# Kernel optimization log

Hardware: AMD Instinct MI355X
Metric: run time of the kernel (lower is better)

## Reference

```python
import jax, jax.numpy as jnp
import numpy as np
from jax import lax

B, X, H, W, C = 4, 32, 8, 128, 32  # batch, frames, height, width, channels (dim)


def setup_inputs() -> dict:
    key = jax.random.key(0)
    k1, k2, k3, k4, k5, k6 = jax.random.split(key, 6)
    return {
        "storage": jax.random.normal(k1, (B, X, H, W, C), jnp.float32),
        "target": jax.random.normal(k2, (B, 1, H, W, C), jnp.float32),
        # Conv3d(dim, 2*dim, kernel=(3,1,1), padding=(1,0,0)) weight/bias
        "w_cross": jax.random.normal(k3, (2 * C, C, 3, 1, 1), jnp.float32) * 0.05,
        "b_cross": jax.random.normal(k4, (2 * C,), jnp.float32) * 0.05,
        # Conv2d(dim, dim, kernel=1) weight (stored as [out, in]) / bias
        "w_q": jax.random.normal(k5, (C, C), jnp.float32) * 0.1,
        "b_q": jax.random.normal(k6, (C,), jnp.float32) * 0.1,
    }


def reference(storage, target, w_cross, b_cross, w_q, b_q):
    # storage [B,X,H,W,C] -> transpose(4,1).transpose(4,2) -> [B,C,X,W,H]
    s = jnp.transpose(storage, (0, 4, 1, 3, 2))
    # target [B,1,H,W,C] -> transpose(4,2) -> [B,1,C,W,H] -> squeeze(1) -> [B,C,W,H]
    t = jnp.transpose(target, (0, 1, 4, 3, 2))[:, 0]

    # Conv3d over the X (depth) axis, kernel (3,1,1), padding (1,0,0)
    out = lax.conv_general_dilated(
        s, w_cross, window_strides=(1, 1, 1),
        padding=((1, 1), (0, 0), (0, 0)),
        dimension_numbers=("NCDHW", "OIDHW", "NCDHW"),
    ) + b_cross[None, :, None, None, None]          # [B,2C,X,W,H]
    s_v, s_k = jnp.split(out, 2, axis=1)            # each [B,C,X,W,H]

    # 1x1 Conv2d query projection
    t_q = jnp.einsum("oc,bcwh->bowh", w_q, t) + b_q[None, :, None, None]  # [B,C,W,H]
    # unsqueeze(1).transpose(2,1).repeat over X -> [B,C,X,W,H]
    t_q = jnp.broadcast_to(t_q[:, :, None], (B, C, X, W, H))

    # Faithful torch .view on contiguous [B,C,X,W,H]: row-major reshape mixes C into last dim
    t_q = t_q.reshape(B, X * W, C * H)
    s_v = s_v.reshape(B, X * W, C * H)
    s_k = jnp.swapaxes(s_k.reshape(B, X * W, C * H), 1, 2)  # [B, C*H, X*W]

    kq = jax.nn.softmax(jnp.einsum("bnc,bcm->bnm", t_q, s_k), axis=-1)  # [B, XW, XW]
    final = jnp.einsum("bnm,bmc->bnc", kq, s_v)                          # [B, XW, C*H]
    return final.reshape(B, X, H, W, C)
```

## Files before the change

### kernel.cpp

```cpp
#include <hip/hip_runtime.h>

typedef unsigned short u16;
typedef unsigned int u32;
typedef __attribute__((ext_vector_type(8))) short s16x8;
typedef __attribute__((ext_vector_type(4))) float f32x4;

#define WS_A      0u
#define WS_B      8388608u
#define WS_C      16777216u
#define WS_D      25165824u
#define WS_E      25427968u
#define WS_LP     25452544u
#define WS_NEEDED 25485312u

__device__ __forceinline__ u16 f2bf(float f){
  u32 u = __float_as_uint(f);
  return (u16)((u + 0x7fffu + ((u >> 16) & 1u)) >> 16);
}

__global__ __launch_bounds__(256) void zero_out_kernel(float* __restrict__ out){
  int t = blockIdx.x * 256 + threadIdx.x;
  ((float4*)out)[t] = make_float4(0.f, 0.f, 0.f, 0.f);
}

__global__ __launch_bounds__(256) void prep_kernel(const float* __restrict__ target,
    const float* __restrict__ w_q, const float* __restrict__ b_q, u16* __restrict__ Qbf,
    const float* __restrict__ w_cross, float* __restrict__ wT){
  int bid = blockIdx.x;
  int tid = threadIdx.x;
  if (bid >= 512){
    int t = (bid - 512) * 256 + tid;
    wT[t] = w_cross[(t & 63) * 96 + (t >> 6)];
    return;
  }
  int wc = bid & 3;
  int cq = (bid >> 2) & 31;
  int b  = bid >> 7;
  int wl = tid & 31, h = tid >> 5;
  int w = wc * 32 + wl;
  float in[32];
  const float4* p = (const float4*)(target + (((size_t)b*8 + h)*128 + w)*32);
  #pragma unroll
  for (int q = 0; q < 8; ++q){
    float4 v = p[q];
    in[q*4+0] = v.x; in[q*4+1] = v.y; in[q*4+2] = v.z; in[q*4+3] = v.w;
  }
  float acc = b_q[cq];
  #pragma unroll
  for (int c = 0; c < 32; ++c) acc += in[c] * w_q[cq*32 + c];
  __shared__ float stg[256];
  stg[wl*8 + h] = acc;
  __syncthreads();
  Qbf[((size_t)b*128 + cq*4 + wc)*256 + tid] = f2bf(stg[tid]);
}

__global__ __launch_bounds__(256, 2) void conv_kernel(const float* __restrict__ storage,
    const float* __restrict__ wT, const float* __restrict__ b_cross,
    u16* __restrict__ Kb, u16* __restrict__ Vb){
  int bid = blockIdx.x;
  int wc  = bid & 3;
  int x   = (bid >> 2) & 31;
  int og2 = (bid >> 7) & 3;
  int b   = bid >> 9;
  int tid = threadIdx.x;
  int wl = tid & 31, h = tid >> 5;
  int w = wc * 32 + wl;
  int obase_ch = og2 * 16;

  float acc[16];
  #pragma unroll
  for (int i = 0; i < 16; ++i) acc[i] = b_cross[obase_ch + i];

  #pragma unroll
  for (int dx = 0; dx < 3; ++dx){
    int xx = x + dx - 1;
    if (xx < 0 || xx > 31) continue;
    float vv[32];
    const float4* p = (const float4*)(storage + ((((size_t)b*32 + xx)*8 + h)*128 + w)*32);
    #pragma unroll
    for (int q = 0; q < 8; ++q){
      float4 v = p[q];
      vv[q*4+0] = v.x; vv[q*4+1] = v.y; vv[q*4+2] = v.z; vv[q*4+3] = v.w;
    }
    #pragma unroll
    for (int c = 0; c < 32; ++c){
      float v = vv[c];
      const float* wp = wT + (c*3 + dx)*64 + obase_ch;
      #pragma unroll
      for (int i = 0; i < 16; ++i) acc[i] = fmaf(v, wp[i], acc[i]);
    }
  }

  int m = wl*8 + h;
  size_t base = ((size_t)b*4096 + (size_t)x*4 + wc)*256 + m;
  if (og2 < 2){
    #pragma unroll
    for (int i = 0; i < 16; ++i)
      Vb[base + (size_t)(obase_ch + i)*32768] = f2bf(acc[i]);
  } else {
    #pragma unroll
    for (int i = 0; i < 16; ++i)
      Kb[base + (size_t)(obase_ch + i - 32)*32768] = f2bf(acc[i]);
  }
}

__global__ __launch_bounds__(256, 2) void flash_kernel(const u16* __restrict__ Qbf,
    const u16* __restrict__ Kb, const u16* __restrict__ Vb,
    float* __restrict__ Opart, float* __restrict__ lpart){
  int kq = blockIdx.x & 15, rb = (blockIdx.x >> 4) & 7, b = blockIdx.x >> 7;
  int tid = threadIdx.x;
  int w = tid >> 6, lane = tid & 63, l15 = lane & 15, quad = lane >> 4;

  __shared__ alignas(16) u16 Vts[256 * 64];
  __shared__ alignas(16) u16 Ps[16 * 64];
  __shared__ float lsumW[64];

  s16x8 qa[8];
  {
    const u16* qp = Qbf + ((size_t)(b*128 + rb*16 + l15))*256 + quad*8;
    #pragma unroll
    for (int ks = 0; ks < 8; ++ks) qa[ks] = *(const s16x8*)(qp + ks*32);
  }

  int jl4 = tid & 15, mseg = tid >> 4;
  const u16* kbase = Kb + ((size_t)(b*4096 + kq*256 + w*16 + l15))*256 + quad*8;
  const u16* vbase = Vb + ((size_t)(b*4096 + kq*256 + jl4*4))*256 + mseg*16;

  s16x8 kr[8];
  #pragma unroll
  for (int ks = 0; ks < 8; ++ks) kr[ks] = *(const s16x8*)(kbase + ks*32);
  u32 kv[4][8];
  #pragma unroll
  for (int kk = 0; kk < 4; ++kk){
    uint4 a = *(const uint4*)(vbase + kk*256);
    uint4 b2 = *(const uint4*)(vbase + kk*256 + 8);
    kv[kk][0]=a.x; kv[kk][1]=a.y; kv[kk][2]=a.z; kv[kk][3]=a.w;
    kv[kk][4]=b2.x; kv[kk][5]=b2.y; kv[kk][6]=b2.z; kv[kk][7]=b2.w;
  }

  float lacc[4] = {0.f, 0.f, 0.f, 0.f};
  f32x4 oc[4];
  #pragma unroll
  for (int mt = 0; mt < 4; ++mt) oc[mt] = (f32x4){0.f,0.f,0.f,0.f};

  #pragma unroll
  for (int it = 0; it < 4; ++it){
    if (it > 0) __syncthreads();

    #pragma unroll
    for (int i = 0; i < 16; ++i){
      int d = i >> 1;
      u32 e0, e1, e2, e3;
      if (i & 1){ e0 = kv[0][d] >> 16;     e1 = kv[1][d] >> 16;
                  e2 = kv[2][d] >> 16;     e3 = kv[3][d] >> 16; }
      else      { e0 = kv[0][d] & 0xffffu; e1 = kv[1][d] & 0xffffu;
                  e2 = kv[2][d] & 0xffffu; e3 = kv[3][d] & 0xffffu; }
      int m = mseg*16 + i;
      int col = (((jl4 >> 1) ^ (m & 7)) << 3) + ((jl4 & 1) << 2);
      *(uint2*)&Vts[m*64 + col] = make_uint2(e0 | (e1 << 16), e2 | (e3 << 16));
    }

    f32x4 s0 = {0.f,0.f,0.f,0.f}, s1 = {0.f,0.f,0.f,0.f};
    #pragma unroll
    for (int ks = 0; ks < 8; ks += 2){
      s0 = __builtin_amdgcn_mfma_f32_16x16x32_bf16(qa[ks],   kr[ks],   s0, 0, 0, 0);
      s1 = __builtin_amdgcn_mfma_f32_16x16x32_bf16(qa[ks+1], kr[ks+1], s1, 0, 0, 0);
    }
    int b8k = w*2 + (l15 >> 3);
    #pragma unroll
    for (int reg = 0; reg < 4; ++reg){
      float sv = fminf(s0[reg] + s1[reg], 80.f);
      float p = __expf(sv);
      int row = quad*4 + reg;
      Ps[row*64 + ((b8k ^ (row & 7)) << 3) + (l15 & 7)] = f2bf(p);
      lacc[reg] += p;
    }

    if (it < 3){
      const u16* vp = vbase + (it+1)*16384;
      #pragma unroll
      for (int kk = 0; kk < 4; ++kk){
        uint4 a = *(const uint4*)(vp + kk*256);
        uint4 b2 = *(const uint4*)(vp + kk*256 + 8);
        kv[kk][0]=a.x; kv[kk][1]=a.y; kv[kk][2]=a.z; kv[kk][3]=a.w;
        kv[kk][4]=b2.x; kv[kk][5]=b2.y; kv[kk][6]=b2.z; kv[kk][7]=b2.w;
      }
    }
    __syncthreads();

    if (it < 3){
      const u16* kp = kbase + (it+1)*16384;
      #pragma unroll
      for (int ks = 0; ks < 8; ++ks) kr[ks] = *(const s16x8*)(kp + ks*32);
    }
    #pragma unroll
    for (int ks2 = 0; ks2 < 2; ++ks2){
      int b8 = ks2*4 + quad;
      s16x8 pb = *(const s16x8*)&Ps[l15*64 + ((b8 ^ (l15 & 7)) << 3)];
      #pragma unroll
      for (int mt = 0; mt < 4; ++mt){
        int mrow = (w*4 + mt)*16 + l15;
        s16x8 af = *(const s16x8*)&Vts[mrow*64 + ((b8 ^ (mrow & 7)) << 3)];
        oc[mt] = __builtin_amdgcn_mfma_f32_16x16x32_bf16(af, pb, oc[mt], 0, 0, 0);
      }
    }
  }

  #pragma unroll
  for (int reg = 0; reg < 4; ++reg){
    float t = lacc[reg];
    t += __shfl_xor(t, 1); t += __shfl_xor(t, 2);
    t += __shfl_xor(t, 4); t += __shfl_xor(t, 8);
    lacc[reg] = t;
  }
  if (l15 == 0){
    #pragma unroll
    for (int reg = 0; reg < 4; ++reg) lsumW[w*16 + quad*4 + reg] = lacc[reg];
  }
  __syncthreads();
  if (tid < 16)
    lpart[(b*16 + kq)*128 + rb*16 + tid] =
        lsumW[tid] + lsumW[16 + tid] + lsumW[32 + tid] + lsumW[48 + tid];
  {
    float* dst = Opart + ((size_t)((b*16 + kq)*128 + rb*16 + l15))*256 + w*64 + quad*4;
    #pragma unroll
    for (int mt = 0; mt < 4; ++mt)
      *(float4*)(dst + mt*16) = make_float4(oc[mt][0], oc[mt][1], oc[mt][2], oc[mt][3]);
  }
}

__global__ __launch_bounds__(256) void combine_kernel(const float* __restrict__ lpart,
    const float* __restrict__ Opart, float* __restrict__ out){
  int r = blockIdx.x & 127, b = blockIdx.x >> 7;
  int m = threadIdx.x;
  float L = 0.f, o = 0.f;
  #pragma unroll
  for (int kq = 0; kq < 16; ++kq){
    L += lpart[(b*16 + kq)*128 + r];
    o += Opart[((size_t)((b*16 + kq)*128 + r))*256 + m];
  }
  o /= L;
  int cq = r >> 2, whi = r & 3;
  size_t obase = ((size_t)b*32 + cq) * 32768;
  #pragma unroll
  for (int hh = 0; hh < 8; ++hh){
    #pragma unroll
    for (int wt = 0; wt < 4; ++wt){
      out[obase + hh*4096 + wt*1024 + whi*256 + m] = o;
    }
  }
}

extern "C" void kernel_launch(void* const* d_in, const int* in_sizes, int n_in,
                              void* d_out, int out_size, void* d_ws, size_t ws_size,
                              hipStream_t stream){
  const float* storage = (const float*)d_in[0];
  const float* target  = (const float*)d_in[1];
  const float* w_cross = (const float*)d_in[2];
  const float* b_cross = (const float*)d_in[3];
  const float* w_q     = (const float*)d_in[4];
  const float* b_q     = (const float*)d_in[5];
  float* out = (float*)d_out;

  if (ws_size < (size_t)WS_NEEDED){
    zero_out_kernel<<<dim3(4096), dim3(256), 0, stream>>>(out);
    return;
  }

  char* ws = (char*)d_ws;
  float* Opart = (float*)(ws + WS_A);
  u16*   Kb    = (u16*)(ws + WS_B);
  u16*   Vb    = (u16*)(ws + WS_C);
  u16*   Qbf   = (u16*)(ws + WS_D);
  float* wT    = (float*)(ws + WS_E);
  float* lpart = (float*)(ws + WS_LP);

  prep_kernel    <<<dim3(536),  dim3(256), 0, stream>>>(target, w_q, b_q, Qbf, w_cross, wT);
  conv_kernel    <<<dim3(2048), dim3(256), 0, stream>>>(storage, wT, b_cross, Kb, Vb);
  flash_kernel   <<<dim3(512),  dim3(256), 0, stream>>>(Qbf, Kb, Vb, Opart, lpart);
  combine_kernel <<<dim3(512),  dim3(256), 0, stream>>>(lpart, Opart, out);
}
```

Before: 135.8 us.

## Fuse four stage kernels into one cooperative persistent kernel with grid syncs

Moves the prep, conv, flash and combine stages into device-function bodies and runs them from a single cooperative mega-kernel. A persistent grid, sized from the occupancy query and capped at 512 blocks, loops over each stage's work units, with grid.sync between stages. This removes three kernel launch boundaries and their idle gaps. In exchange it adds grid-wide barrier cost, an occupancy query on the host at every call, possible lower parallelism in the conv stage (2048 units on at most 512 blocks), and register pressure from merging all stages into one kernel. The old four-kernel path stays as a fallback if the cooperative launch fails.

```diff
diff --git a/kernel.cpp b/kernel.cpp
--- a/kernel.cpp
+++ b/kernel.cpp
@@ -1,4 +1,7 @@
 #include <hip/hip_runtime.h>
+#include <hip/hip_cooperative_groups.h>
+
+namespace cg = cooperative_groups;
 
 typedef unsigned short u16;
 typedef unsigned int u32;
@@ -23,16 +26,10 @@
   ((float4*)out)[t] = make_float4(0.f, 0.f, 0.f, 0.f);
 }
 
-__global__ __launch_bounds__(256) void prep_kernel(const float* __restrict__ target,
-    const float* __restrict__ w_q, const float* __restrict__ b_q, u16* __restrict__ Qbf,
-    const float* __restrict__ w_cross, float* __restrict__ wT){
-  int bid = blockIdx.x;
-  int tid = threadIdx.x;
-  if (bid >= 512){
-    int t = (bid - 512) * 256 + tid;
-    wT[t] = w_cross[(t & 63) * 96 + (t >> 6)];
-    return;
-  }
+
+__device__ __forceinline__ void qproj_body(int bid, int tid,
+    const float* __restrict__ target, const float* __restrict__ w_q,
+    const float* __restrict__ b_q, u16* __restrict__ Qbf, float* stg){
   int wc = bid & 3;
   int cq = (bid >> 2) & 31;
   int b  = bid >> 7;
@@ -48,21 +45,18 @@
   float acc = b_q[cq];
   #pragma unroll
   for (int c = 0; c < 32; ++c) acc += in[c] * w_q[cq*32 + c];
-  __shared__ float stg[256];
   stg[wl*8 + h] = acc;
   __syncthreads();
   Qbf[((size_t)b*128 + cq*4 + wc)*256 + tid] = f2bf(stg[tid]);
 }
 
-__global__ __launch_bounds__(256, 2) void conv_kernel(const float* __restrict__ storage,
-    const float* __restrict__ wT, const float* __restrict__ b_cross,
-    u16* __restrict__ Kb, u16* __restrict__ Vb){
-  int bid = blockIdx.x;
+__device__ __forceinline__ void conv_body(int bid, int tid,
+    const float* __restrict__ storage, const float* __restrict__ wT,
+    const float* __restrict__ b_cross, u16* __restrict__ Kb, u16* __restrict__ Vb){
   int wc  = bid & 3;
   int x   = (bid >> 2) & 31;
   int og2 = (bid >> 7) & 3;
   int b   = bid >> 9;
-  int tid = threadIdx.x;
   int wl = tid & 31, h = tid >> 5;
   int w = wc * 32 + wl;
   int obase_ch = og2 * 16;
@@ -104,16 +98,16 @@
   }
 }
 
-__global__ __launch_bounds__(256, 2) void flash_kernel(const u16* __restrict__ Qbf,
-    const u16* __restrict__ Kb, const u16* __restrict__ Vb,
-    float* __restrict__ Opart, float* __restrict__ lpart){
-  int kq = blockIdx.x & 15, rb = (blockIdx.x >> 4) & 7, b = blockIdx.x >> 7;
-  int tid = threadIdx.x;
+__device__ __forceinline__ void flash_body(int bid, int tid,
+    const u16* __restrict__ Qbf, const u16* __restrict__ Kb,
+    const u16* __restrict__ Vb, float* __restrict__ Opart,
+    float* __restrict__ lpart, char* smem){
+  u16*   Vts   = (u16*)smem;
+  u16*   Ps    = (u16*)(smem + 32768);
+  float* lsumW = (float*)(smem + 34816);
+
+  int kq = bid & 15, rb = (bid >> 4) & 7, b = bid >> 7;
   int w = tid >> 6, lane = tid & 63, l15 = lane & 15, quad = lane >> 4;
-
-  __shared__ alignas(16) u16 Vts[256 * 64];
-  __shared__ alignas(16) u16 Ps[16 * 64];
-  __shared__ float lsumW[64];
 
   s16x8 qa[8];
   {
@@ -145,7 +139,7 @@
 
   #pragma unroll
   for (int it = 0; it < 4; ++it){
-    if (it > 0) __syncthreads();
+    __syncthreads();
 
     #pragma unroll
     for (int i = 0; i < 16; ++i){
@@ -213,6 +207,7 @@
     t += __shfl_xor(t, 4); t += __shfl_xor(t, 8);
     lacc[reg] = t;
   }
+  __syncthreads();
   if (l15 == 0){
     #pragma unroll
     for (int reg = 0; reg < 4; ++reg) lsumW[w*16 + quad*4 + reg] = lacc[reg];
@@ -229,10 +224,11 @@
   }
 }
 
-__global__ __launch_bounds__(256) void combine_kernel(const float* __restrict__ lpart,
-    const float* __restrict__ Opart, float* __restrict__ out){
-  int r = blockIdx.x & 127, b = blockIdx.x >> 7;
-  int m = threadIdx.x;
+__device__ __forceinline__ void combine_body(int bid, int tid,
+    const float* __restrict__ lpart, const float* __restrict__ Opart,
+    float* __restrict__ out){
+  int r = bid & 127, b = bid >> 7;
+  int m = tid;
   float L = 0.f, o = 0.f;
   #pragma unroll
   for (int kq = 0; kq < 16; ++kq){
@@ -249,6 +245,81 @@
       out[obase + hh*4096 + wt*1024 + whi*256 + m] = o;
     }
   }
+}
+
+
+__global__ __launch_bounds__(256) void prep_kernel(const float* __restrict__ target,
+    const float* __restrict__ w_q, const float* __restrict__ b_q, u16* __restrict__ Qbf,
+    const float* __restrict__ w_cross, float* __restrict__ wT){
+  __shared__ float stg[256];
+  int bid = blockIdx.x, tid = threadIdx.x;
+  if (bid >= 512){
+    int t = (bid - 512) * 256 + tid;
+    wT[t] = w_cross[(t & 63) * 96 + (t >> 6)];
+    return;
+  }
+  qproj_body(bid, tid, target, w_q, b_q, Qbf, stg);
+}
+
+__global__ __launch_bounds__(256, 2) void conv_kernel(const float* __restrict__ storage,
+    const float* __restrict__ wT, const float* __restrict__ b_cross,
+    u16* __restrict__ Kb, u16* __restrict__ Vb){
+  conv_body(blockIdx.x, threadIdx.x, storage, wT, b_cross, Kb, Vb);
+}
+
+__global__ __launch_bounds__(256, 2) void flash_kernel(const u16* __restrict__ Qbf,
+    const u16* __restrict__ Kb, const u16* __restrict__ Vb,
+    float* __restrict__ Opart, float* __restrict__ lpart){
+  __shared__ alignas(16) char smem[35072];
+  flash_body(blockIdx.x, threadIdx.x, Qbf, Kb, Vb, Opart, lpart, smem);
+}
+
+__global__ __launch_bounds__(256) void combine_kernel(const float* __restrict__ lpart,
+    const float* __restrict__ Opart, float* __restrict__ out){
+  combine_body(blockIdx.x, threadIdx.x, lpart, Opart, out);
+}
+
+
+__global__ __launch_bounds__(256, 2) void mega_kernel(
+    const float* __restrict__ storage, const float* __restrict__ target,
+    const float* __restrict__ w_cross, const float* __restrict__ b_cross,
+    const float* __restrict__ w_q, const float* __restrict__ b_q,
+    float* __restrict__ out, char* __restrict__ ws){
+  cg::grid_group grid = cg::this_grid();
+
+  float* Opart = (float*)(ws + WS_A);
+  u16*   Kb    = (u16*)(ws + WS_B);
+  u16*   Vb    = (u16*)(ws + WS_C);
+  u16*   Qbf   = (u16*)(ws + WS_D);
+  float* wT    = (float*)(ws + WS_E);
+  float* lpart = (float*)(ws + WS_LP);
+
+  __shared__ alignas(16) char smem[35072];
+
+  int tid = threadIdx.x;
+  int G = gridDim.x;
+
+  for (int u = blockIdx.x; u < 536; u += G){
+    if (u >= 512){
+      int t = (u - 512)*256 + tid;
+      wT[t] = w_cross[(t & 63) * 96 + (t >> 6)];
+    } else {
+      qproj_body(u, tid, target, w_q, b_q, Qbf, (float*)smem);
+    }
+    __syncthreads();
+  }
+  grid.sync();
+
+  for (int u = blockIdx.x; u < 2048; u += G)
+    conv_body(u, tid, storage, wT, b_cross, Kb, Vb);
+  grid.sync();
+
+  for (int u = blockIdx.x; u < 512; u += G)
+    flash_body(u, tid, Qbf, Kb, Vb, Opart, lpart, smem);
+  grid.sync();
+
+  for (int u = blockIdx.x; u < 512; u += G)
+    combine_body(u, tid, lpart, Opart, out);
 }
 
 extern "C" void kernel_launch(void* const* d_in, const int* in_sizes, int n_in,
@@ -261,22 +332,37 @@
   const float* w_q     = (const float*)d_in[4];
   const float* b_q     = (const float*)d_in[5];
   float* out = (float*)d_out;
+  char* ws = (char*)d_ws;
 
   if (ws_size < (size_t)WS_NEEDED){
     zero_out_kernel<<<dim3(4096), dim3(256), 0, stream>>>(out);
     return;
   }
 
-  char* ws = (char*)d_ws;
-  float* Opart = (float*)(ws + WS_A);
-  u16*   Kb    = (u16*)(ws + WS_B);
-  u16*   Vb    = (u16*)(ws + WS_C);
-  u16*   Qbf   = (u16*)(ws + WS_D);
-  float* wT    = (float*)(ws + WS_E);
-  float* lpart = (float*)(ws + WS_LP);
-
-  prep_kernel    <<<dim3(536),  dim3(256), 0, stream>>>(target, w_q, b_q, Qbf, w_cross, wT);
-  conv_kernel    <<<dim3(2048), dim3(256), 0, stream>>>(storage, wT, b_cross, Kb, Vb);
-  flash_kernel   <<<dim3(512),  dim3(256), 0, stream>>>(Qbf, Kb, Vb, Opart, lpart);
-  combine_kernel <<<dim3(512),  dim3(256), 0, stream>>>(lpart, Opart, out);
-}
+  bool coop_ok = false;
+  int occ = 0;
+  hipError_t qerr = hipOccupancyMaxActiveBlocksPerMultiprocessor(
+      &occ, (const void*)mega_kernel, 256, 0);
+  if (qerr == hipSuccess && occ > 0){
+    int grid = occ * 256;
+    if (grid > 512) grid = 512;
+    void* args[] = {(void*)&storage, (void*)&target, (void*)&w_cross, (void*)&b_cross,
+                    (void*)&w_q, (void*)&b_q, (void*)&out, (void*)&ws};
+    hipError_t lerr = hipLaunchCooperativeKernel((const void*)mega_kernel,
+                                                 dim3(grid), dim3(256), args, 0, stream);
+    coop_ok = (lerr == hipSuccess);
+  }
+  if (!coop_ok){
+    (void)hipGetLastError();
+    float* Opart = (float*)(ws + WS_A);
+    u16*   Kb    = (u16*)(ws + WS_B);
+    u16*   Vb    = (u16*)(ws + WS_C);
+    u16*   Qbf   = (u16*)(ws + WS_D);
+    float* wT    = (float*)(ws + WS_E);
+    float* lpart = (float*)(ws + WS_LP);
+    prep_kernel    <<<dim3(536),  dim3(256), 0, stream>>>(target, w_q, b_q, Qbf, w_cross, wT);
+    conv_kernel    <<<dim3(2048), dim3(256), 0, stream>>>(storage, wT, b_cross, Kb, Vb);
+    flash_kernel   <<<dim3(512),  dim3(256), 0, stream>>>(Qbf, Kb, Vb, Opart, lpart);
+    combine_kernel <<<dim3(512),  dim3(256), 0, stream>>>(lpart, Opart, out);
+  }
+}
```

Result: slower. 309.9 us (+128.1%).

## Fuse query projection into conv kernel and drop weight transpose pass

Applied to the files above, without the earlier changes.

Merges the prep kernel (query projection plus conv-weight transpose) into the conv kernel, so the first 512 blocks also compute Q, and reads w_cross directly in its original layout instead of a transposed copy. Each thread now loads all three input frames up front (96 registers) and loops over output channels without unrolling, storing each result as soon as it is computed. This removes one kernel launch and the wT workspace, at the cost of higher register pressure and strided weight reads. A __syncthreads is also added before the lsum shared-memory write in the flash kernel.

```diff
diff --git a/kernel.cpp b/kernel.cpp
--- a/kernel.cpp
+++ b/kernel.cpp
@@ -9,7 +9,6 @@
 #define WS_B      8388608u
 #define WS_C      16777216u
 #define WS_D      25165824u
-#define WS_E      25427968u
 #define WS_LP     25452544u
 #define WS_NEEDED 25485312u
 
@@ -23,84 +22,77 @@
   ((float4*)out)[t] = make_float4(0.f, 0.f, 0.f, 0.f);
 }
 
-__global__ __launch_bounds__(256) void prep_kernel(const float* __restrict__ target,
-    const float* __restrict__ w_q, const float* __restrict__ b_q, u16* __restrict__ Qbf,
-    const float* __restrict__ w_cross, float* __restrict__ wT){
+__global__ __launch_bounds__(256, 2) void convq_kernel(const float* __restrict__ storage,
+    const float* __restrict__ target, const float* __restrict__ w_cross,
+    const float* __restrict__ b_cross, const float* __restrict__ w_q,
+    const float* __restrict__ b_q, u16* __restrict__ Kb, u16* __restrict__ Vb,
+    u16* __restrict__ Qbf){
   int bid = blockIdx.x;
   int tid = threadIdx.x;
-  if (bid >= 512){
-    int t = (bid - 512) * 256 + tid;
-    wT[t] = w_cross[(t & 63) * 96 + (t >> 6)];
-    return;
-  }
-  int wc = bid & 3;
-  int cq = (bid >> 2) & 31;
-  int b  = bid >> 7;
   int wl = tid & 31, h = tid >> 5;
-  int w = wc * 32 + wl;
-  float in[32];
-  const float4* p = (const float4*)(target + (((size_t)b*8 + h)*128 + w)*32);
-  #pragma unroll
-  for (int q = 0; q < 8; ++q){
-    float4 v = p[q];
-    in[q*4+0] = v.x; in[q*4+1] = v.y; in[q*4+2] = v.z; in[q*4+3] = v.w;
-  }
-  float acc = b_q[cq];
-  #pragma unroll
-  for (int c = 0; c < 32; ++c) acc += in[c] * w_q[cq*32 + c];
-  __shared__ float stg[256];
-  stg[wl*8 + h] = acc;
-  __syncthreads();
-  Qbf[((size_t)b*128 + cq*4 + wc)*256 + tid] = f2bf(stg[tid]);
-}
-
-__global__ __launch_bounds__(256, 2) void conv_kernel(const float* __restrict__ storage,
-    const float* __restrict__ wT, const float* __restrict__ b_cross,
-    u16* __restrict__ Kb, u16* __restrict__ Vb){
-  int bid = blockIdx.x;
-  int wc  = bid & 3;
-  int x   = (bid >> 2) & 31;
-  int og2 = (bid >> 7) & 3;
-  int b   = bid >> 9;
-  int tid = threadIdx.x;
-  int wl = tid & 31, h = tid >> 5;
-  int w = wc * 32 + wl;
-  int obase_ch = og2 * 16;
-
-  float acc[16];
-  #pragma unroll
-  for (int i = 0; i < 16; ++i) acc[i] = b_cross[obase_ch + i];
-
-  #pragma unroll
-  for (int dx = 0; dx < 3; ++dx){
-    int xx = x + dx - 1;
-    if (xx < 0 || xx > 31) continue;
-    float vv[32];
-    const float4* p = (const float4*)(storage + ((((size_t)b*32 + xx)*8 + h)*128 + w)*32);
+
+  if (bid < 512){
+    int wc = bid & 3;
+    int cq = (bid >> 2) & 31;
+    int b  = bid >> 7;
+    int w = wc * 32 + wl;
+    float in[32];
+    const float4* p = (const float4*)(target + (((size_t)b*8 + h)*128 + w)*32);
     #pragma unroll
     for (int q = 0; q < 8; ++q){
       float4 v = p[q];
-      vv[q*4+0] = v.x; vv[q*4+1] = v.y; vv[q*4+2] = v.z; vv[q*4+3] = v.w;
-    }
-    #pragma unroll
-    for (int c = 0; c < 32; ++c){
-      float v = vv[c];
-      const float* wp = wT + (c*3 + dx)*64 + obase_ch;
-      #pragma unroll
-      for (int i = 0; i < 16; ++i) acc[i] = fmaf(v, wp[i], acc[i]);
-    }
-  }
-
-  int m = wl*8 + h;
-  size_t base = ((size_t)b*4096 + (size_t)x*4 + wc)*256 + m;
-  if (og2 < 2){
-    #pragma unroll
-    for (int i = 0; i < 16; ++i)
-      Vb[base + (size_t)(obase_ch + i)*32768] = f2bf(acc[i]);
-  } else {
-    #pragma unroll
-    for (int i = 0; i < 16; ++i)
-      Kb[base + (size_t)(obase_ch + i - 32)*32768] = f2bf(acc[i]);
+      in[q*4+0] = v.x; in[q*4+1] = v.y; in[q*4+2] = v.z; in[q*4+3] = v.w;
+    }
+    float acc = b_q[cq];
+    #pragma unroll
+    for (int c = 0; c < 32; ++c) acc += in[c] * w_q[cq*32 + c];
+    __shared__ float stg[256];
+    stg[wl*8 + h] = acc;
+    __syncthreads();
+    Qbf[((size_t)b*128 + cq*4 + wc)*256 + tid] = f2bf(stg[tid]);
+  }
+
+  {
+    int wc  = bid & 3;
+    int x   = (bid >> 2) & 31;
+    int og2 = (bid >> 7) & 3;
+    int b   = bid >> 9;
+    int w = wc * 32 + wl;
+    int obase_ch = og2 * 16;
+
+    float vv[3][32];
+    #pragma unroll
+    for (int dx = 0; dx < 3; ++dx){
+      int xx = x + dx - 1;
+      if (xx < 0 || xx > 31){
+        #pragma unroll
+        for (int c = 0; c < 32; ++c) vv[dx][c] = 0.f;
+      } else {
+        const float4* p = (const float4*)(storage + ((((size_t)b*32 + xx)*8 + h)*128 + w)*32);
+        #pragma unroll
+        for (int q = 0; q < 8; ++q){
+          float4 v = p[q];
+          vv[dx][q*4+0] = v.x; vv[dx][q*4+1] = v.y;
+          vv[dx][q*4+2] = v.z; vv[dx][q*4+3] = v.w;
+        }
+      }
+    }
+
+    int m = wl*8 + h;
+    size_t base = ((size_t)b*4096 + (size_t)x*4 + wc)*256 + m;
+    #pragma unroll 1
+    for (int i = 0; i < 16; ++i){
+      int o = obase_ch + i;
+      const float* wp = w_cross + o*96;
+      float acc = b_cross[o];
+      #pragma unroll
+      for (int c = 0; c < 32; ++c){
+        acc += vv[0][c]*wp[c*3+0] + vv[1][c]*wp[c*3+1] + vv[2][c]*wp[c*3+2];
+      }
+      u16 r = f2bf(acc);
+      if (og2 < 2) Vb[base + (size_t)o*32768] = r;
+      else         Kb[base + (size_t)(o - 32)*32768] = r;
+    }
   }
 }
 
@@ -213,6 +205,7 @@
     t += __shfl_xor(t, 4); t += __shfl_xor(t, 8);
     lacc[reg] = t;
   }
+  __syncthreads();
   if (l15 == 0){
     #pragma unroll
     for (int reg = 0; reg < 4; ++reg) lsumW[w*16 + quad*4 + reg] = lacc[reg];
@@ -272,11 +265,10 @@
   u16*   Kb    = (u16*)(ws + WS_B);
   u16*   Vb    = (u16*)(ws + WS_C);
   u16*   Qbf   = (u16*)(ws + WS_D);
-  float* wT    = (float*)(ws + WS_E);
   float* lpart = (float*)(ws + WS_LP);
 
-  prep_kernel    <<<dim3(536),  dim3(256), 0, stream>>>(target, w_q, b_q, Qbf, w_cross, wT);
-  conv_kernel    <<<dim3(2048), dim3(256), 0, stream>>>(storage, wT, b_cross, Kb, Vb);
+  convq_kernel   <<<dim3(2048), dim3(256), 0, stream>>>(storage, target, w_cross,
+                                                        b_cross, w_q, b_q, Kb, Vb, Qbf);
   flash_kernel   <<<dim3(512),  dim3(256), 0, stream>>>(Qbf, Kb, Vb, Opart, lpart);
   combine_kernel <<<dim3(512),  dim3(256), 0, stream>>>(lpart, Opart, out);
 }
```

After: 161.7 us. 1.19x slower.
